# Optimization experiments

Hardware: AMD Instinct MI355X
Metric: run time of the kernel (lower is better)

Reference implementation:

```python
import jax, jax.numpy as jnp
import numpy as np

GRID_SIZE = 5      # KANLinear default
SPLINE_ORDER = 3   # KANLinear default
N_CONVS = 16
K = 3              # kernel side
P = K * K          # in_features of each KANLinear
G = GRID_SIZE + SPLINE_ORDER  # number of spline coefficients per input


def make_grid():
    # grid_range=[-1,1]: h = 2/grid_size; extended by spline_order on each side
    h = 2.0 / GRID_SIZE
    return jnp.arange(-SPLINE_ORDER, GRID_SIZE + SPLINE_ORDER + 1, dtype=jnp.float32) * h - 1.0  # (12,)


def b_splines(x, grid):
    # Cox-de Boor recursion, faithful to efficient-kan KANLinear.b_splines.
    # x: (N, P) -> bases: (N, P, G). Grid is identical across the P inputs.
    x = x[..., None]  # (N, P, 1)
    bases = ((x >= grid[:-1]) & (x < grid[1:])).astype(x.dtype)  # (N, P, 11)
    for k in range(1, SPLINE_ORDER + 1):
        left = (x - grid[:-(k + 1)]) / (grid[k:-1] - grid[:-(k + 1)]) * bases[..., :-1]
        right = (grid[k + 1:] - x) / (grid[k + 1:] - grid[1:-k]) * bases[..., 1:]
        bases = left + right
    return bases  # (N, P, G)


def setup_inputs() -> dict:
    key = jax.random.key(0)
    ks = jax.random.split(key, 6)
    B, H, W = 32, 256, 256
    x = jax.random.normal(ks[0], (B, 1, H, W), dtype=jnp.float32)
    # Per-conv KANLinear(in=9, out=1) params, stacked over the 16 convs.
    base_w = jax.random.normal(ks[1], (N_CONVS, P), dtype=jnp.float32) / np.sqrt(P).astype(np.float32)
    spline_w = jax.random.normal(ks[2], (N_CONVS, P, G), dtype=jnp.float32) * 0.1
    spline_scaler = jax.random.normal(ks[3], (N_CONVS, P), dtype=jnp.float32) / np.sqrt(P).astype(np.float32)
    # restore: Conv2d(16, 1, 3, padding=1)
    restore_w = jax.random.normal(ks[4], (1, N_CONVS, K, K), dtype=jnp.float32) / np.sqrt(N_CONVS * P).astype(np.float32)
    restore_b = jax.random.normal(ks[5], (1,), dtype=jnp.float32) * 0.01
    return {"x": x, "base_w": base_w, "spline_w": spline_w,
            "spline_scaler": spline_scaler, "restore_w": restore_w, "restore_b": restore_b}


def reference(x, base_w, spline_w, spline_scaler, restore_w, restore_b):
    B, C, H, W = x.shape  # C == 1
    # Unfold 3x3 patches, stride 1, padding 1 -> (B, H, W, 9), row-major kernel order
    xp = jnp.pad(x, ((0, 0), (0, 0), (1, 1), (1, 1)))
    patches = jnp.stack([xp[:, 0, i:i + H, j:j + W] for i in range(K) for j in range(K)], axis=-1)
    flat = patches.reshape(-1, P)  # (N, 9), N = B*H*W
    bases = b_splines(flat, make_grid())  # (N, 9, G) -- shared across all 16 convs
    scaled_spline_w = spline_w * spline_scaler[..., None]  # (16, 9, G)
    # KANLinear: base (SiLU -> linear) + spline (bases -> linear), per conv
    out = jnp.einsum('np,cp->nc', jax.nn.silu(flat), base_w) \
        + jnp.einsum('npg,cpg->nc', bases, scaled_spline_w)  # (N, 16)
    feat = out.reshape(B, H, W, N_CONVS).transpose(0, 3, 1, 2)  # (B, 16, H, W)
    y = jax.lax.conv_general_dilated(feat, restore_w, (1, 1), [(1, 1), (1, 1)],
                                     dimension_numbers=('NCHW', 'OIHW', 'NCHW'))
    return y + restore_b[None, :, None, None]  # (B, 1, H, W)
```

## Files before the change

kernel.cpp:

```cpp
#include <hip/hip_runtime.h>
#include <math.h>

#define IMG 256
#define TS 32
#define EBASE 736

typedef _Float16 half_t;
typedef _Float16 half2_t __attribute__((ext_vector_type(2)));

__device__ __forceinline__ half2_t bc_h2(unsigned int u) {
    union { unsigned int u; half2_t h; } c; c.u = u; return c.h;
}
__device__ __forceinline__ unsigned int bc_u(half2_t h) {
    union { unsigned int u; half2_t h; } c; c.h = h; return c.u;
}

__device__ __forceinline__ float dot2(half2_t a, half2_t b, float c) {
#if __has_builtin(__builtin_amdgcn_fdot2)
    return __builtin_amdgcn_fdot2(a, b, c, false);
#else
    return fmaf((float)a.x, (float)b.x, fmaf((float)a.y, (float)b.y, c));
#endif
}

__global__ __launch_bounds__(1024) void kkan_precompute(
    const float* __restrict__ bw, const float* __restrict__ sw,
    const float* __restrict__ sc, const float* __restrict__ rw,
    float* __restrict__ ws)
{
    __shared__ float sF[729];
    const int tid = threadIdx.x;
    if (tid < 729) {
        const int u = tid / 81, p = (tid / 9) % 9, j = tid % 9;
        float f = 0.f;
        for (int c = 0; c < 16; ++c) {
            const float w = (j < 8) ? sw[(c * 9 + p) * 8 + j] * sc[c * 9 + p]
                                    : bw[c * 9 + p];
            f += rw[c * 9 + u] * w;
        }
        sF[tid] = f;
        ws[tid] = f;
    }
    __syncthreads();
    unsigned int* wse = (unsigned int*)ws + EBASE;
    if (tid < 200) {
        const int jp = tid / 40, rem = tid % 40, sy = rem / 8, sx = rem % 8;
        unsigned int val = 0u;
        if (sx < 5) {
            float e0 = 0.f, e1 = 0.f;
            for (int uy = 0; uy < 3; ++uy) {
                const int py = sy - uy; if (py < 0 || py > 2) continue;
                for (int ux = 0; ux < 3; ++ux) {
                    const int px = sx - ux; if (px < 0 || px > 2) continue;
                    const float* fb = &sF[((uy * 3 + ux) * 9 + (py * 3 + px)) * 9];
                    e0 += fb[2 * jp];
                    if (2 * jp + 1 < 9) e1 += fb[2 * jp + 1];
                }
            }
            val = bc_u(half2_t{(half_t)e0, (half_t)e1});
        }
        wse[tid] = val;
    }
}

__device__ __forceinline__ void phi_store(unsigned int* s_phi, int pix, float v) {
    const int yy = pix / 36, xx = pix - yy * 36;
    const float sil = v / (1.f + __expf(-v));
    float u0 = (v + 2.2f) * 2.5f;
    u0 = fminf(fmaxf(u0, 0.f), 11.f);
    float c[12];
    #pragma unroll
    for (int m = 0; m < 12; ++m) {
        const float d = fmaxf(u0 - (float)m, 0.f);
        c[m] = d * d * d;
    }
    float ph[8];
    #pragma unroll
    for (int j = 0; j < 8; ++j)
        ph[j] = (c[j] - 4.f * c[j + 1] + 6.f * c[j + 2]
                 - 4.f * c[j + 3] + c[j + 4]) * (1.f / 6.f);
    unsigned int* dst = &s_phi[yy * 36 + xx];
    dst[0 * 1296] = bc_u(half2_t{(half_t)ph[0], (half_t)ph[1]});
    dst[1 * 1296] = bc_u(half2_t{(half_t)ph[2], (half_t)ph[3]});
    dst[2 * 1296] = bc_u(half2_t{(half_t)ph[4], (half_t)ph[5]});
    dst[3 * 1296] = bc_u(half2_t{(half_t)ph[6], (half_t)ph[7]});
    dst[4 * 1296] = bc_u(half2_t{(half_t)sil,   (half_t)0.f});
}

__device__ __forceinline__ float phi_at(const unsigned int* s_phi, int j, int r, int c) {
    const half2_t h = bc_h2(s_phi[(j >> 1) * 1296 + r * 36 + c]);
    return (j & 1) ? (float)h.y : (float)h.x;
}

__global__ __launch_bounds__(256, 6) void kkan_fused(
    const float* __restrict__ x, const float* __restrict__ ws,
    const float* __restrict__ rb, float* __restrict__ out)
{
    __shared__ __align__(16) unsigned int s_phi[5 * 36 * 36];

    const int tid = threadIdx.x;
    const int gx0 = blockIdx.x * TS, gy0 = blockIdx.y * TS, b = blockIdx.z;
    const float* xb = x + (size_t)b * (IMG * IMG);

    float vx[6];
    #pragma unroll
    for (int it = 0; it < 6; ++it) {
        const int pix = tid + it * 256;
        float v = 0.f;
        if (it < 5 || tid < 16) {
            const int yy = pix / 36, xx = pix - yy * 36;
            const int gy = gy0 - 2 + yy, gx = gx0 - 2 + xx;
            if ((unsigned)gy < (unsigned)IMG && (unsigned)gx < (unsigned)IMG)
                v = xb[gy * IMG + gx];
        }
        vx[it] = v;
    }

    #pragma unroll
    for (int it = 0; it < 5; ++it) phi_store(s_phi, tid + it * 256, vx[it]);
    if (tid < 16) phi_store(s_phi, tid + 1280, vx[5]);
    __syncthreads();

    const int ly = tid >> 3;
    const int lx0 = (tid & 7) * 4;
    const unsigned int* Eu = (const unsigned int*)ws + EBASE;

    float aA0 = 0.f, aB0 = 0.f, aA1 = 0.f, aB1 = 0.f;
    float aA2 = 0.f, aB2 = 0.f, aA3 = 0.f, aB3 = 0.f;

    #pragma unroll
    for (int jp = 0; jp < 5; ++jp) {
        #pragma unroll
        for (int sy = 0; sy < 5; ++sy) {
            const unsigned int* eb = &Eu[(jp * 5 + sy) * 8];
            const half2_t e0 = bc_h2(eb[0]);
            const half2_t e1 = bc_h2(eb[1]);
            const half2_t e2 = bc_h2(eb[2]);
            const half2_t e3 = bc_h2(eb[3]);
            const half2_t e4 = bc_h2(eb[4]);
            const unsigned int* prow = &s_phi[(jp * 36 + ly + sy) * 36 + lx0];
            const uint4 pa = *(const uint4*)prow;
            const uint4 pb = *(const uint4*)(prow + 4);
            const half2_t q0 = bc_h2(pa.x), q1 = bc_h2(pa.y);
            const half2_t q2 = bc_h2(pa.z), q3 = bc_h2(pa.w);
            const half2_t q4 = bc_h2(pb.x), q5 = bc_h2(pb.y);
            const half2_t q6 = bc_h2(pb.z), q7 = bc_h2(pb.w);
            aA0 = dot2(q0, e0, dot2(q2, e2, dot2(q4, e4, aA0)));
            aB0 = dot2(q1, e1, dot2(q3, e3, aB0));
            aA1 = dot2(q1, e0, dot2(q3, e2, dot2(q5, e4, aA1)));
            aB1 = dot2(q2, e1, dot2(q4, e3, aB1));
            aA2 = dot2(q2, e0, dot2(q4, e2, dot2(q6, e4, aA2)));
            aB2 = dot2(q3, e1, dot2(q5, e3, aB2));
            aA3 = dot2(q3, e0, dot2(q5, e2, dot2(q7, e4, aA3)));
            aB3 = dot2(q4, e1, dot2(q6, e3, aB3));
        }
    }
    float a0 = aA0 + aB0, a1 = aA1 + aB1, a2 = aA2 + aB2, a3 = aA3 + aB3;

    const int gy  = gy0 + ly;
    const int gxb = gx0 + lx0;
    if (gy < 2 || gy > 253 || gxb < 2 || gxb > 250) {
        #pragma unroll
        for (int i = 0; i < 4; ++i) {
            const int gx = gxb + i;
            float corr = 0.f;
            for (int uy = 0; uy < 3; ++uy) {
                const int qy = gy + uy - 1;
                for (int ux = 0; ux < 3; ++ux) {
                    const int qx = gx + ux - 1;
                    if ((unsigned)qy < (unsigned)IMG && (unsigned)qx < (unsigned)IMG)
                        continue;
                    for (int p = 0; p < 9; ++p) {
                        const int ry = ly + uy + (p / 3);
                        const int rx = lx0 + i + ux + (p % 3);
                        const float* fp = &ws[((uy * 3 + ux) * 9 + p) * 9];
                        for (int jj = 0; jj < 9; ++jj)
                            corr += fp[jj] * phi_at(s_phi, jj, ry, rx);
                    }
                }
            }
            if (i == 0) a0 -= corr;
            else if (i == 1) a1 -= corr;
            else if (i == 2) a2 -= corr;
            else a3 -= corr;
        }
    }

    const float rbv = rb[0];
    float4 o4; o4.x = a0 + rbv; o4.y = a1 + rbv; o4.z = a2 + rbv; o4.w = a3 + rbv;
    *(float4*)&out[(size_t)b * (IMG * IMG) + gy * IMG + gxb] = o4;
}

extern "C" void kernel_launch(void* const* d_in, const int* in_sizes, int n_in,
                              void* d_out, int out_size, void* d_ws, size_t ws_size,
                              hipStream_t stream) {
    const float* x             = (const float*)d_in[0];
    const float* base_w        = (const float*)d_in[1];
    const float* spline_w      = (const float*)d_in[2];
    const float* spline_scaler = (const float*)d_in[3];
    const float* restore_w     = (const float*)d_in[4];
    const float* restore_b     = (const float*)d_in[5];
    float* out = (float*)d_out;
    float* ws  = (float*)d_ws;

    kkan_precompute<<<dim3(1), dim3(1024), 0, stream>>>(
        base_w, spline_w, spline_scaler, restore_w, ws);

    kkan_fused<<<dim3(8, 8, 32), dim3(256), 0, stream>>>(x, ws, restore_b, out);
}
```

Baseline: 46.00 us.

## Process four images per block with double-buffered phi tiles and prefetch

Result: slower. 96.77 us (+110.4%).

```diff
diff --git a/kernel.cpp b/kernel.cpp
--- a/kernel.cpp
+++ b/kernel.cpp
@@ -92,17 +92,9 @@
     return (j & 1) ? (float)h.y : (float)h.x;
 }
 
-__global__ __launch_bounds__(256, 6) void kkan_fused(
-    const float* __restrict__ x, const float* __restrict__ ws,
-    const float* __restrict__ rb, float* __restrict__ out)
-{
-    __shared__ __align__(16) unsigned int s_phi[5 * 36 * 36];
-
-    const int tid = threadIdx.x;
-    const int gx0 = blockIdx.x * TS, gy0 = blockIdx.y * TS, b = blockIdx.z;
-    const float* xb = x + (size_t)b * (IMG * IMG);
-
-    float vx[6];
+__device__ __forceinline__ void load_halo(float* v6, const float* __restrict__ xb,
+                                          int gx0, int gy0, int tid)
+{
     #pragma unroll
     for (int it = 0; it < 6; ++it) {
         const int pix = tid + it * 256;
@@ -113,23 +105,23 @@
             if ((unsigned)gy < (unsigned)IMG && (unsigned)gx < (unsigned)IMG)
                 v = xb[gy * IMG + gx];
         }
-        vx[it] = v;
-    }
-
-    #pragma unroll
-    for (int it = 0; it < 5; ++it) phi_store(s_phi, tid + it * 256, vx[it]);
-    if (tid < 16) phi_store(s_phi, tid + 1280, vx[5]);
-    __syncthreads();
-
-    const int ly = tid >> 3;
-    const int lx0 = (tid & 7) * 4;
-    const unsigned int* Eu = (const unsigned int*)ws + EBASE;
-
+        v6[it] = v;
+    }
+}
+
+template <bool DOPHI>
+__device__ __forceinline__ void conv_phase(
+    const unsigned int* __restrict__ cb, unsigned int* pb, const float* vx,
+    const unsigned int* __restrict__ Eu, const float* __restrict__ wsF,
+    const int tid, const int ly, const int lx0, const int gy, const int gxb,
+    const bool edge, const float rbv, float* __restrict__ outp)
+{
     float aA0 = 0.f, aB0 = 0.f, aA1 = 0.f, aB1 = 0.f;
     float aA2 = 0.f, aB2 = 0.f, aA3 = 0.f, aB3 = 0.f;
 
     #pragma unroll
     for (int jp = 0; jp < 5; ++jp) {
+        if (DOPHI) phi_store(pb, tid + jp * 256, vx[jp]);
         #pragma unroll
         for (int sy = 0; sy < 5; ++sy) {
             const unsigned int* eb = &Eu[(jp * 5 + sy) * 8];
@@ -138,13 +130,13 @@
             const half2_t e2 = bc_h2(eb[2]);
             const half2_t e3 = bc_h2(eb[3]);
             const half2_t e4 = bc_h2(eb[4]);
-            const unsigned int* prow = &s_phi[(jp * 36 + ly + sy) * 36 + lx0];
+            const unsigned int* prow = &cb[(jp * 36 + ly + sy) * 36 + lx0];
             const uint4 pa = *(const uint4*)prow;
-            const uint4 pb = *(const uint4*)(prow + 4);
+            const uint4 pq = *(const uint4*)(prow + 4);
             const half2_t q0 = bc_h2(pa.x), q1 = bc_h2(pa.y);
             const half2_t q2 = bc_h2(pa.z), q3 = bc_h2(pa.w);
-            const half2_t q4 = bc_h2(pb.x), q5 = bc_h2(pb.y);
-            const half2_t q6 = bc_h2(pb.z), q7 = bc_h2(pb.w);
+            const half2_t q4 = bc_h2(pq.x), q5 = bc_h2(pq.y);
+            const half2_t q6 = bc_h2(pq.z), q7 = bc_h2(pq.w);
             aA0 = dot2(q0, e0, dot2(q2, e2, dot2(q4, e4, aA0)));
             aB0 = dot2(q1, e1, dot2(q3, e3, aB0));
             aA1 = dot2(q1, e0, dot2(q3, e2, dot2(q5, e4, aA1)));
@@ -155,11 +147,11 @@
             aB3 = dot2(q4, e1, dot2(q6, e3, aB3));
         }
     }
+    if (DOPHI) { if (tid < 16) phi_store(pb, tid + 1280, vx[5]); }
+
     float a0 = aA0 + aB0, a1 = aA1 + aB1, a2 = aA2 + aB2, a3 = aA3 + aB3;
 
-    const int gy  = gy0 + ly;
-    const int gxb = gx0 + lx0;
-    if (gy < 2 || gy > 253 || gxb < 2 || gxb > 250) {
+    if (edge) {
         #pragma unroll
         for (int i = 0; i < 4; ++i) {
             const int gx = gxb + i;
@@ -173,9 +165,9 @@
                     for (int p = 0; p < 9; ++p) {
                         const int ry = ly + uy + (p / 3);
                         const int rx = lx0 + i + ux + (p % 3);
-                        const float* fp = &ws[((uy * 3 + ux) * 9 + p) * 9];
+                        const float* fp = &wsF[((uy * 3 + ux) * 9 + p) * 9];
                         for (int jj = 0; jj < 9; ++jj)
-                            corr += fp[jj] * phi_at(s_phi, jj, ry, rx);
+                            corr += fp[jj] * phi_at(cb, jj, ry, rx);
                     }
                 }
             }
@@ -186,9 +178,54 @@
         }
     }
 
+    float4 o4; o4.x = a0 + rbv; o4.y = a1 + rbv; o4.z = a2 + rbv; o4.w = a3 + rbv;
+    *(float4*)&outp[gy * IMG + gxb] = o4;
+}
+
+__global__ __launch_bounds__(256, 3) void kkan_fused(
+    const float* __restrict__ x, const float* __restrict__ ws,
+    const float* __restrict__ rb, float* __restrict__ out)
+{
+    __shared__ __align__(16) unsigned int s_buf[12960];
+    unsigned int* b0 = s_buf;
+    unsigned int* b1 = s_buf + 6480;
+
+    const int tid = threadIdx.x;
+    const int gx0 = blockIdx.x * TS, gy0 = blockIdx.y * TS, zb = blockIdx.z;
+    const int ly  = tid >> 3;
+    const int lx0 = (tid & 7) * 4;
+    const int gy  = gy0 + ly;
+    const int gxb = gx0 + lx0;
+    const bool edge = (gy < 2 || gy > 253 || gxb < 2 || gxb > 250);
+    const unsigned int* Eu = (const unsigned int*)ws + EBASE;
     const float rbv = rb[0];
-    float4 o4; o4.x = a0 + rbv; o4.y = a1 + rbv; o4.z = a2 + rbv; o4.w = a3 + rbv;
-    *(float4*)&out[(size_t)b * (IMG * IMG) + gy * IMG + gxb] = o4;
+    const size_t imsz = (size_t)IMG * IMG;
+
+    float vxA[6], vxB[6];
+    load_halo(vxA, x + (size_t)zb * imsz, gx0, gy0, tid);
+    load_halo(vxB, x + (size_t)(zb + 8) * imsz, gx0, gy0, tid);
+
+    #pragma unroll
+    for (int it = 0; it < 5; ++it) phi_store(b0, tid + it * 256, vxA[it]);
+    if (tid < 16) phi_store(b0, tid + 1280, vxA[5]);
+    __syncthreads();
+
+    load_halo(vxA, x + (size_t)(zb + 16) * imsz, gx0, gy0, tid);
+    conv_phase<true>(b0, b1, vxB, Eu, ws, tid, ly, lx0, gy, gxb, edge, rbv,
+                     out + (size_t)zb * imsz);
+    __syncthreads();
+
+    load_halo(vxB, x + (size_t)(zb + 24) * imsz, gx0, gy0, tid);
+    conv_phase<true>(b1, b0, vxA, Eu, ws, tid, ly, lx0, gy, gxb, edge, rbv,
+                     out + (size_t)(zb + 8) * imsz);
+    __syncthreads();
+
+    conv_phase<true>(b0, b1, vxB, Eu, ws, tid, ly, lx0, gy, gxb, edge, rbv,
+                     out + (size_t)(zb + 16) * imsz);
+    __syncthreads();
+
+    conv_phase<false>(b1, nullptr, nullptr, Eu, ws, tid, ly, lx0, gy, gxb, edge, rbv,
+                      out + (size_t)(zb + 24) * imsz);
 }
 
 extern "C" void kernel_launch(void* const* d_in, const int* in_sizes, int n_in,
@@ -206,5 +243,5 @@
     kkan_precompute<<<dim3(1), dim3(1024), 0, stream>>>(
         base_w, spline_w, spline_scaler, restore_w, ws);
 
-    kkan_fused<<<dim3(8, 8, 32), dim3(256), 0, stream>>>(x, ws, restore_b, out);
-}
+    kkan_fused<<<dim3(8, 8, 8), dim3(256), 0, stream>>>(x, ws, restore_b, out);
+}
```

## Split spline-basis computation into separate pass writing packed fp16 phi to workspace

Applied to the files above, without the earlier changes.

After: 83.32 us. 1.81x slower.

```diff
diff --git a/kernel.cpp b/kernel.cpp
--- a/kernel.cpp
+++ b/kernel.cpp
@@ -4,6 +4,8 @@
 #define IMG 256
 #define TS 32
 #define EBASE 736
+#define EBASE2 1024
+#define PHI_BASE 1280
 
 typedef _Float16 half_t;
 typedef _Float16 half2_t __attribute__((ext_vector_type(2)));
@@ -40,9 +42,35 @@
         }
         sF[tid] = f;
         ws[tid] = f;
+    } else if (tid < 729 + 288) {
+        ((unsigned int*)ws)[EBASE + tid - 729] = 0u;
     }
     __syncthreads();
     unsigned int* wse = (unsigned int*)ws + EBASE;
+    if (tid < 45) {
+        const int j = tid / 5, sy = tid % 5;
+        float e[5];
+        for (int sx = 0; sx < 5; ++sx) {
+            float acc = 0.f;
+            for (int uy = 0; uy < 3; ++uy) {
+                const int py = sy - uy; if (py < 0 || py > 2) continue;
+                for (int ux = 0; ux < 3; ++ux) {
+                    const int px = sx - ux; if (px < 0 || px > 2) continue;
+                    acc += sF[((uy * 3 + ux) * 9 + (py * 3 + px)) * 9 + j];
+                }
+            }
+            e[sx] = acc;
+        }
+        unsigned int* oe = wse + j * 32 + sy * 3;
+        oe[0] = bc_u(half2_t{(half_t)e[0], (half_t)e[1]});
+        oe[1] = bc_u(half2_t{(half_t)e[2], (half_t)e[3]});
+        oe[2] = bc_u(half2_t{(half_t)e[4], (half_t)0.f});
+        unsigned int* oo = wse + j * 32 + 16 + sy * 3;
+        oo[0] = bc_u(half2_t{(half_t)0.f, (half_t)e[0]});
+        oo[1] = bc_u(half2_t{(half_t)e[1], (half_t)e[2]});
+        oo[2] = bc_u(half2_t{(half_t)e[3], (half_t)e[4]});
+    }
+    unsigned int* wse2 = (unsigned int*)ws + EBASE2;
     if (tid < 200) {
         const int jp = tid / 40, rem = tid % 40, sy = rem / 8, sx = rem % 8;
         unsigned int val = 0u;
@@ -59,11 +87,159 @@
             }
             val = bc_u(half2_t{(half_t)e0, (half_t)e1});
         }
-        wse[tid] = val;
-    }
-}
-
-__device__ __forceinline__ void phi_store(unsigned int* s_phi, int pix, float v) {
+        wse2[tid] = val;
+    }
+}
+
+__global__ __launch_bounds__(256) void kkan_phi(
+    const float* __restrict__ x, unsigned int* __restrict__ phi)
+{
+    const int t = blockIdx.x * 256 + threadIdx.x;
+    const float4 xa = ((const float4*)x)[2 * t];
+    const float4 xb = ((const float4*)x)[2 * t + 1];
+    const float v[8] = {xa.x, xa.y, xa.z, xa.w, xb.x, xb.y, xb.z, xb.w};
+    unsigned int w[36];
+    #pragma unroll
+    for (int k = 0; k < 4; ++k) {
+        float ph[2][9];
+        #pragma unroll
+        for (int e = 0; e < 2; ++e) {
+            const float vv = v[2 * k + e];
+            float u0 = (vv + 2.2f) * 2.5f;
+            u0 = fminf(fmaxf(u0, 0.f), 11.f);
+            float c[12];
+            #pragma unroll
+            for (int m = 0; m < 12; ++m) {
+                const float d = fmaxf(u0 - (float)m, 0.f);
+                c[m] = d * d * d;
+            }
+            #pragma unroll
+            for (int j = 0; j < 8; ++j)
+                ph[e][j] = (c[j] - 4.f * c[j + 1] + 6.f * c[j + 2]
+                            - 4.f * c[j + 3] + c[j + 4]) * (1.f / 6.f);
+            ph[e][8] = vv / (1.f + __expf(-vv));
+        }
+        #pragma unroll
+        for (int j = 0; j < 9; ++j)
+            w[k * 9 + j] = bc_u(half2_t{(half_t)ph[0][j], (half_t)ph[1][j]});
+    }
+    uint4* dst = (uint4*)(phi + (size_t)t * 36);
+    #pragma unroll
+    for (int q = 0; q < 9; ++q) {
+        uint4 o; o.x = w[4 * q]; o.y = w[4 * q + 1];
+        o.z = w[4 * q + 2]; o.w = w[4 * q + 3];
+        dst[q] = o;
+    }
+}
+
+__global__ __launch_bounds__(256, 4) void kkan_conv(
+    const unsigned int* __restrict__ phi, const float* __restrict__ ws,
+    const float* __restrict__ rb, float* __restrict__ out)
+{
+    __shared__ __align__(16) unsigned int s_phi[9 * 36 * 20];
+
+    const int tid = threadIdx.x;
+    const int gx0 = blockIdx.x * TS, gy0 = blockIdx.y * TS, bz = blockIdx.z;
+    const int gxp0 = blockIdx.x * 16 - 1;
+
+    const unsigned int c148  = bc_u(half2_t{(half_t)(1.f / 48.f), (half_t)(1.f / 48.f)});
+    const unsigned int c2348 = bc_u(half2_t{(half_t)(23.f / 48.f), (half_t)(23.f / 48.f)});
+
+    for (int i = tid; i < 5832; i += 256) {
+        const int row = i / 162;
+        const int rem = i - row * 162;
+        const int xp  = rem / 9;
+        const int j   = rem - xp * 9;
+        const int grow = gy0 - 2 + row;
+        const int gxp  = gxp0 + xp;
+        unsigned int wv;
+        if ((unsigned)grow < 256u && (unsigned)gxp < 128u) {
+            wv = phi[(((size_t)bz * 256 + grow) * 128 + gxp) * 9 + j];
+        } else {
+            wv = (j == 2 || j == 5) ? c148 : ((j == 3 || j == 4) ? c2348 : 0u);
+        }
+        s_phi[j * 720 + row * 20 + xp] = wv;
+    }
+    __syncthreads();
+
+    const half_t* sp = (const half_t*)s_phi;
+    const int ly  = tid >> 3;
+    const int lx0 = (tid & 7) * 4;
+    const uint4* Eg = (const uint4*)((const unsigned int*)ws + EBASE);
+
+    float aA0 = 0.f, aB0 = 0.f, aC0 = 0.f;
+    float aA1 = 0.f, aB1 = 0.f, aC1 = 0.f;
+    float aA2 = 0.f, aB2 = 0.f, aC2 = 0.f;
+    float aA3 = 0.f, aB3 = 0.f, aC3 = 0.f;
+
+    #pragma unroll
+    for (int j = 0; j < 9; ++j) {
+        unsigned int ej[32];
+        #pragma unroll
+        for (int q = 0; q < 8; ++q) {
+            const uint4 t4 = Eg[j * 8 + q];
+            ej[q * 4 + 0] = t4.x; ej[q * 4 + 1] = t4.y;
+            ej[q * 4 + 2] = t4.z; ej[q * 4 + 3] = t4.w;
+        }
+        #pragma unroll
+        for (int sy = 0; sy < 5; ++sy) {
+            const half2_t ev0 = bc_h2(ej[sy * 3 + 0]);
+            const half2_t ev1 = bc_h2(ej[sy * 3 + 1]);
+            const half2_t ev2 = bc_h2(ej[sy * 3 + 2]);
+            const half2_t od0 = bc_h2(ej[16 + sy * 3 + 0]);
+            const half2_t od1 = bc_h2(ej[16 + sy * 3 + 1]);
+            const half2_t od2 = bc_h2(ej[16 + sy * 3 + 2]);
+            const uint2* pp = (const uint2*)(sp + j * 1440 + (ly + sy) * 40 + lx0);
+            const uint2 ph0 = pp[0], ph1 = pp[1];
+            const half2_t P0 = bc_h2(ph0.x), P1 = bc_h2(ph0.y);
+            const half2_t P2 = bc_h2(ph1.x), P3 = bc_h2(ph1.y);
+            aA0 = dot2(P0, ev0, aA0); aB0 = dot2(P1, ev1, aB0); aC0 = dot2(P2, ev2, aC0);
+            aA1 = dot2(P0, od0, aA1); aB1 = dot2(P1, od1, aB1); aC1 = dot2(P2, od2, aC1);
+            aA2 = dot2(P1, ev0, aA2); aB2 = dot2(P2, ev1, aB2); aC2 = dot2(P3, ev2, aC2);
+            aA3 = dot2(P1, od0, aA3); aB3 = dot2(P2, od1, aB3); aC3 = dot2(P3, od2, aC3);
+        }
+    }
+
+    float a0 = aA0 + aB0 + aC0;
+    float a1 = aA1 + aB1 + aC1;
+    float a2 = aA2 + aB2 + aC2;
+    float a3 = aA3 + aB3 + aC3;
+
+    const int gy  = gy0 + ly;
+    const int gxb = gx0 + lx0;
+    if (gy < 2 || gy > 253 || gxb < 2 || gxb > 250) {
+        #pragma unroll
+        for (int i = 0; i < 4; ++i) {
+            const int gx = gxb + i;
+            float corr = 0.f;
+            for (int uy = 0; uy < 3; ++uy) {
+                const int qy = gy + uy - 1;
+                for (int ux = 0; ux < 3; ++ux) {
+                    const int qx = gx + ux - 1;
+                    if ((unsigned)qy < (unsigned)IMG && (unsigned)qx < (unsigned)IMG)
+                        continue;
+                    for (int p = 0; p < 9; ++p) {
+                        const int ry = ly + uy + (p / 3);
+                        const int rx = lx0 + i + ux + (p % 3);
+                        const float* fp = &ws[((uy * 3 + ux) * 9 + p) * 9];
+                        for (int jj = 0; jj < 9; ++jj)
+                            corr += fp[jj] * (float)sp[jj * 1440 + ry * 40 + rx];
+                    }
+                }
+            }
+            if (i == 0) a0 -= corr;
+            else if (i == 1) a1 -= corr;
+            else if (i == 2) a2 -= corr;
+            else a3 -= corr;
+        }
+    }
+
+    const float rbv = rb[0];
+    float4 o4; o4.x = a0 + rbv; o4.y = a1 + rbv; o4.z = a2 + rbv; o4.w = a3 + rbv;
+    *(float4*)&out[(size_t)bz * (IMG * IMG) + gy * IMG + gxb] = o4;
+}
+
+__device__ __forceinline__ void phi_store_fb(unsigned int* s_phi, int pix, float v) {
     const int yy = pix / 36, xx = pix - yy * 36;
     const float sil = v / (1.f + __expf(-v));
     float u0 = (v + 2.2f) * 2.5f;
@@ -87,12 +263,12 @@
     dst[4 * 1296] = bc_u(half2_t{(half_t)sil,   (half_t)0.f});
 }
 
-__device__ __forceinline__ float phi_at(const unsigned int* s_phi, int j, int r, int c) {
+__device__ __forceinline__ float phi_at_fb(const unsigned int* s_phi, int j, int r, int c) {
     const half2_t h = bc_h2(s_phi[(j >> 1) * 1296 + r * 36 + c]);
     return (j & 1) ? (float)h.y : (float)h.x;
 }
 
-__global__ __launch_bounds__(256, 6) void kkan_fused(
+__global__ __launch_bounds__(256, 6) void kkan_fused_fb(
     const float* __restrict__ x, const float* __restrict__ ws,
     const float* __restrict__ rb, float* __restrict__ out)
 {
@@ -115,15 +291,14 @@
         }
         vx[it] = v;
     }
-
-    #pragma unroll
-    for (int it = 0; it < 5; ++it) phi_store(s_phi, tid + it * 256, vx[it]);
-    if (tid < 16) phi_store(s_phi, tid + 1280, vx[5]);
+    #pragma unroll
+    for (int it = 0; it < 5; ++it) phi_store_fb(s_phi, tid + it * 256, vx[it]);
+    if (tid < 16) phi_store_fb(s_phi, tid + 1280, vx[5]);
     __syncthreads();
 
-    const int ly = tid >> 3;
+    const int ly  = tid >> 3;
     const int lx0 = (tid & 7) * 4;
-    const unsigned int* Eu = (const unsigned int*)ws + EBASE;
+    const unsigned int* Eu = (const unsigned int*)ws + EBASE2;
 
     float aA0 = 0.f, aB0 = 0.f, aA1 = 0.f, aB1 = 0.f;
     float aA2 = 0.f, aB2 = 0.f, aA3 = 0.f, aB3 = 0.f;
@@ -175,7 +350,7 @@
                         const int rx = lx0 + i + ux + (p % 3);
                         const float* fp = &ws[((uy * 3 + ux) * 9 + p) * 9];
                         for (int jj = 0; jj < 9; ++jj)
-                            corr += fp[jj] * phi_at(s_phi, jj, ry, rx);
+                            corr += fp[jj] * phi_at_fb(s_phi, jj, ry, rx);
                     }
                 }
             }
@@ -206,5 +381,12 @@
     kkan_precompute<<<dim3(1), dim3(1024), 0, stream>>>(
         base_w, spline_w, spline_scaler, restore_w, ws);
 
-    kkan_fused<<<dim3(8, 8, 32), dim3(256), 0, stream>>>(x, ws, restore_b, out);
-}
+    const size_t need = (size_t)PHI_BASE * 4 + (size_t)32 * 256 * 128 * 9 * 4;
+    if (ws_size >= need) {
+        unsigned int* phi = (unsigned int*)ws + PHI_BASE;
+        kkan_phi<<<dim3(1024), dim3(256), 0, stream>>>(x, phi);
+        kkan_conv<<<dim3(8, 8, 32), dim3(256), 0, stream>>>(phi, ws, restore_b, out);
+    } else {
+        kkan_fused_fb<<<dim3(8, 8, 32), dim3(256), 0, stream>>>(x, ws, restore_b, out);
+    }
+}
```
